# Kernel tuning notes

Hardware: AMD Instinct MI355X
Metric: run time of the kernel (lower is better)

The kernel has to match this reference:

```python
import jax, jax.numpy as jnp
import numpy as np

B, S, N_STATE, N_HEAD = 8, 4096, 1024, 16
N_FREQ = 10000.0
H_DIM = N_STATE // N_HEAD          # 64
N_ROTS = H_DIM // 2                # 32


def setup_inputs() -> dict:
    key = jax.random.key(0)
    k1, k2, k3, k4, k5 = jax.random.split(key, 5)
    x = jax.random.normal(k1, (B, S, N_STATE), dtype=jnp.float32)
    # rotation angles (module inits to zeros; small random values exercise the math)
    thetas = jax.random.normal(k2, (N_ROTS,), dtype=jnp.float32) * 0.1
    # r_pairs.long() in torch -> integer plane indices; ensure i != j
    i = jax.random.randint(k3, (N_ROTS,), 0, H_DIM)
    off = jax.random.randint(k4, (N_ROTS,), 1, H_DIM)
    j = (i + off) % H_DIM
    r_pairs = jnp.stack([i, j], axis=-1).astype(jnp.int32)
    theta_scale = jnp.ones((1,), dtype=jnp.float32)
    # r_matrix inits to identity; add small noise so it is non-trivial
    r_matrix = jnp.eye(H_DIM, dtype=jnp.float32) + 0.01 * jax.random.normal(k5, (H_DIM, H_DIM), dtype=jnp.float32)
    inv_freq = 1.0 / (N_FREQ ** (jnp.arange(0, H_DIM, 2, dtype=jnp.float32) / H_DIM))
    return {"x": x, "thetas": thetas, "theta_scale": theta_scale,
            "r_matrix": r_matrix, "inv_freq": inv_freq,
            "r_pairs": r_pairs, "n_head": N_HEAD}


def reference(x, thetas, theta_scale, r_matrix, inv_freq, r_pairs, n_head):
    b, s, n_state = x.shape
    h_dim = n_state // n_head
    x2d = x.reshape(-1, h_dim)  # [B*S*H, h_dim]
    angles = thetas * theta_scale[0]

    # Sequential Givens plane rotations: x @ G(i,j,theta) only touches columns i, j.
    def step(carry, inp):
        theta, ij = inp
        i, j = ij[0], ij[1]
        c, sn = jnp.cos(theta), jnp.sin(theta)
        xi = carry[:, i]
        xj = carry[:, j]
        carry = carry.at[:, i].set(xi * c + xj * sn)
        carry = carry.at[:, j].set(-xi * sn + xj * c)
        return carry, None

    x2d, _ = jax.lax.scan(step, x2d, (angles, r_pairs))
    x2d = x2d @ r_matrix
    xh = x2d.reshape(b, s, n_head, h_dim)

    # RoPE-style sin/cos mix
    pos = jnp.arange(s, dtype=jnp.float32)
    sinu = pos[:, None] * inv_freq[None, :]          # [s, h_dim//2]
    sin = jnp.sin(sinu)[None, :, None, :]
    cos = jnp.cos(sinu)[None, :, None, :]
    x1, x2 = xh[..., ::2], xh[..., 1::2]
    out = jnp.concatenate([x1 * cos - x2 * sin, x1 * sin + x2 * cos], axis=-1)
    return out.reshape(b, s, n_state)
```

## Files before the change

### kernel.cpp

```cpp
#include <hip/hip_runtime.h>
#include <cstdint>
#include <cstddef>

#define S_LEN   4096
#define NROT    32
#define NGRP    8192

typedef __attribute__((ext_vector_type(8))) short  short8x;
typedef __attribute__((ext_vector_type(4))) float  floatx4;

__device__ __host__ inline unsigned short f2bf(float f) {
  union { float f; unsigned u; } c; c.f = f;
  unsigned u = c.u;
  return (unsigned short)((u + 0x7fffu + ((u >> 16) & 1u)) >> 16);
}
__device__ inline float bf2f(unsigned short h) {
  union { unsigned u; float f; } c; c.u = ((unsigned)h) << 16;
  return c.f;
}

__global__ void setup_kernel(const float* __restrict__ thetas,
                             const float* __restrict__ theta_scale,
                             const float* __restrict__ r_matrix,
                             const int*   __restrict__ r_pairs,
                             const float* __restrict__ inv_freq,
                             uint4* __restrict__ Bfrag,
                             float* __restrict__ cosT,
                             float* __restrict__ sinT) {
  if (blockIdx.x < 512) {
    int idx = blockIdx.x * 256 + threadIdx.x;
    int s = idx >> 5;
    int f = idx & 31;
    float ang = (float)s * inv_freq[f];
    cosT[idx] = cosf(ang);
    sinT[idx] = sinf(ang);
    return;
  }
  __shared__ float C[64 * 65];
  __shared__ float Mm[64 * 64];
  int tid = threadIdx.x;
  if (tid < 64) {
    for (int c = 0; c < 64; ++c) C[tid * 65 + c] = (tid == c) ? 1.0f : 0.0f;
    float sc = theta_scale[0];
    for (int q = 0; q < NROT; ++q) {
      float th = thetas[q] * sc;
      float cs = cosf(th), sn = sinf(th);
      int i = r_pairs[2 * q], j = r_pairs[2 * q + 1];
      float xi = C[tid * 65 + i];
      float xj = C[tid * 65 + j];
      C[tid * 65 + i] =  xi * cs + xj * sn;
      C[tid * 65 + j] = -xi * sn + xj * cs;
    }
  }
  __syncthreads();
  for (int o = tid; o < 64 * 64; o += 256) {
    int t = o >> 6, c = o & 63;
    float a = 0.0f;
    for (int k = 0; k < 64; ++k) a = fmaf(C[t * 65 + k], r_matrix[k * 64 + c], a);
    Mm[o] = a;
  }
  __syncthreads();
  for (int e = tid; e < 16 * 64; e += 256) {
    int f = e >> 6, l = e & 63;
    int hl = f & 1, ks = (f >> 1) & 1, nt = f >> 2;
    int col = nt * 16 + (l & 15);
    unsigned short w[8];
    for (int j = 0; j < 8; ++j) {
      int k = ks * 32 + (l >> 4) * 8 + j;
      float m = Mm[k * 64 + col];
      unsigned short h = f2bf(m);
      if (hl == 0) w[j] = h;
      else         w[j] = f2bf(m - bf2f(h));
    }
    uint4 pk;
    pk.x = (unsigned)w[0] | ((unsigned)w[1] << 16);
    pk.y = (unsigned)w[2] | ((unsigned)w[3] << 16);
    pk.z = (unsigned)w[4] | ((unsigned)w[5] << 16);
    pk.w = (unsigned)w[6] | ((unsigned)w[7] << 16);
    Bfrag[e] = pk;
  }
}

__global__ __launch_bounds__(256)
void rotary_main(const float* __restrict__ x,
                 const uint4* __restrict__ Bfrag,
                 const float* __restrict__ cosT,
                 const float* __restrict__ sinT,
                 float* __restrict__ out) {
  __shared__ float obuf[4][1024];
  const int tid  = threadIdx.x;
  const int lane = tid & 63;
  const int wid  = tid >> 6;
  const int g    = blockIdx.x * 4 + wid;

  const short8x* Bp = (const short8x*)Bfrag;

  const int lr  = lane & 15;
  const int lk  = lane >> 4;
  const int dq  = lr >> 1;
  const int par = lane & 1;

  const float* xg = x + (size_t)g * 4096;
  float* og = out + (size_t)g * 4096;
  float* ob = &obuf[wid][0];

  floatx4 a[2][4];
  #define LOAD_A(mt, sl)                                                  \
    { const float* xr = xg + (size_t)((mt) * 16 + lr) * 64 + lk * 8;      \
      a[sl][0] = *(const floatx4*)(xr);                                   \
      a[sl][1] = *(const floatx4*)(xr + 4);                               \
      a[sl][2] = *(const floatx4*)(xr + 32);                              \
      a[sl][3] = *(const floatx4*)(xr + 36); }

  LOAD_A(0, 0)

  #pragma unroll
  for (int mt = 0; mt < 4; ++mt) {
    const int cur = mt & 1;
    short8x Ah0, Al0, Ah1, Al1;
    #pragma unroll
    for (int i = 0; i < 8; ++i) {
      float v0 = (i < 4) ? a[cur][0][i] : a[cur][1][i - 4];
      float v1 = (i < 4) ? a[cur][2][i] : a[cur][3][i - 4];
      unsigned short h0 = f2bf(v0);
      unsigned short h1 = f2bf(v1);
      Ah0[i] = (short)h0; Al0[i] = (short)f2bf(v0 - bf2f(h0));
      Ah1[i] = (short)h1; Al1[i] = (short)f2bf(v1 - bf2f(h1));
    }
    if (mt < 3) LOAD_A(mt + 1, (mt + 1) & 1)

    const int spos = (g * 4 + mt) & (S_LEN - 1);
    const float* ct = cosT + spos * 32;
    const float* st = sinT + spos * 32;

    #pragma unroll
    for (int nt = 0; nt < 4; ++nt) {
      short8x b0 = Bp[(nt * 4 + 0) * 64 + lane];
      short8x b1 = Bp[(nt * 4 + 1) * 64 + lane];
      short8x b2 = Bp[(nt * 4 + 2) * 64 + lane];
      short8x b3 = Bp[(nt * 4 + 3) * 64 + lane];

      floatx4 acc0 = {0.f, 0.f, 0.f, 0.f};
      floatx4 acc1 = {0.f, 0.f, 0.f, 0.f};
      acc0 = __builtin_amdgcn_mfma_f32_16x16x32_bf16(Ah0, b0, acc0, 0, 0, 0);
      acc1 = __builtin_amdgcn_mfma_f32_16x16x32_bf16(Ah1, b2, acc1, 0, 0, 0);
      acc0 = __builtin_amdgcn_mfma_f32_16x16x32_bf16(Ah0, b1, acc0, 0, 0, 0);
      acc1 = __builtin_amdgcn_mfma_f32_16x16x32_bf16(Ah1, b3, acc1, 0, 0, 0);
      acc0 = __builtin_amdgcn_mfma_f32_16x16x32_bf16(Al0, b0, acc0, 0, 0, 0);
      acc1 = __builtin_amdgcn_mfma_f32_16x16x32_bf16(Al1, b2, acc1, 0, 0, 0);

      const float cv = ct[nt * 8 + dq];
      const float sv = st[nt * 8 + dq];
      const int colout = par ? (32 + nt * 8 + dq) : (nt * 8 + dq);
      #pragma unroll
      for (int r = 0; r < 4; ++r) {
        float v = acc0[r] + acc1[r];
        float p = __shfl_xor(v, 1, 64);
        float o = par ? fmaf(p, sv, v * cv)
                      : fmaf(v, cv, -(p * sv));
        ob[(lk * 4 + r) * 64 + (colout ^ (lk << 3))] = o;
      }
    }

    asm volatile("s_waitcnt lgkmcnt(0)" ::: "memory");
    #pragma unroll
    for (int q = 0; q < 4; ++q) {
      const float* rp = ob + q * 256 + lk * 64 + ((lr * 4) ^ (q << 3));
      floatx4 vr = *(const floatx4*)rp;
      *(floatx4*)(og + (size_t)(mt * 16 + q * 4 + lk) * 64 + lr * 4) = vr;
    }
  }
  #undef LOAD_A
}

extern "C" void kernel_launch(void* const* d_in, const int* in_sizes, int n_in,
                              void* d_out, int out_size, void* d_ws, size_t ws_size,
                              hipStream_t stream) {
  const float* x           = (const float*)d_in[0];
  const float* thetas      = (const float*)d_in[1];
  const float* theta_scale = (const float*)d_in[2];
  const float* r_matrix    = (const float*)d_in[3];
  const float* inv_freq    = (const float*)d_in[4];
  const int*   r_pairs     = (const int*)d_in[5];

  uint4* Bfrag = (uint4*)d_ws;
  float* cosT  = (float*)d_ws + 4096;
  float* sinT  = cosT + S_LEN * 32;
  float* outp  = (float*)d_out;

  setup_kernel<<<513, 256, 0, stream>>>(thetas, theta_scale, r_matrix, r_pairs,
                                        inv_freq, Bfrag, cosT, sinT);
  rotary_main<<<NGRP / 4, 256, 0, stream>>>(x, Bfrag, cosT, sinT, outp);
}
```

Measured before the change: 82.23 us.

## Hoist B fragments into registers, double work per wave, interleave cos/sin table

Loads all 16 B-matrix MFMA fragments into registers once per wave instead of reloading them on every tile. Each wave now processes two 64-row groups (eight tiles), which halves the grid and amortizes the B loads. The cos and sin tables are merged into one float2 array so each lookup is a single load, and launch bounds request 3 blocks per SM. The cost is higher register pressure from 16 short8 fragments held in registers, and fewer blocks in flight for latency hiding in a memory-bound kernel.

New measurement: 91.33 us. 11.1% more time.

```diff
diff --git a/kernel.cpp b/kernel.cpp
--- a/kernel.cpp
+++ b/kernel.cpp
@@ -25,15 +25,13 @@
                              const int*   __restrict__ r_pairs,
                              const float* __restrict__ inv_freq,
                              uint4* __restrict__ Bfrag,
-                             float* __restrict__ cosT,
-                             float* __restrict__ sinT) {
+                             float2* __restrict__ csT) {
   if (blockIdx.x < 512) {
     int idx = blockIdx.x * 256 + threadIdx.x;
     int s = idx >> 5;
     int f = idx & 31;
     float ang = (float)s * inv_freq[f];
-    cosT[idx] = cosf(ang);
-    sinT[idx] = sinf(ang);
+    csT[idx] = make_float2(cosf(ang), sinf(ang));
     return;
   }
   __shared__ float C[64 * 65];
@@ -81,42 +79,43 @@
   }
 }
 
-__global__ __launch_bounds__(256)
+__global__ __launch_bounds__(256, 3)
 void rotary_main(const float* __restrict__ x,
                  const uint4* __restrict__ Bfrag,
-                 const float* __restrict__ cosT,
-                 const float* __restrict__ sinT,
+                 const float2* __restrict__ csT,
                  float* __restrict__ out) {
   __shared__ float obuf[4][1024];
   const int tid  = threadIdx.x;
   const int lane = tid & 63;
   const int wid  = tid >> 6;
-  const int g    = blockIdx.x * 4 + wid;
+  const int w    = blockIdx.x * 4 + wid;
 
   const short8x* Bp = (const short8x*)Bfrag;
+  short8x Bf[16];
+  #pragma unroll
+  for (int f = 0; f < 16; ++f) Bf[f] = Bp[f * 64 + lane];
 
   const int lr  = lane & 15;
   const int lk  = lane >> 4;
   const int dq  = lr >> 1;
   const int par = lane & 1;
 
-  const float* xg = x + (size_t)g * 4096;
-  float* og = out + (size_t)g * 4096;
   float* ob = &obuf[wid][0];
 
   floatx4 a[2][4];
-  #define LOAD_A(mt, sl)                                                  \
-    { const float* xr = xg + (size_t)((mt) * 16 + lr) * 64 + lk * 8;      \
-      a[sl][0] = *(const floatx4*)(xr);                                   \
-      a[sl][1] = *(const floatx4*)(xr + 4);                               \
-      a[sl][2] = *(const floatx4*)(xr + 32);                              \
+  #define LOAD_A(t, sl)                                                        \
+    { const float* xr = x + (size_t)(w * 2 + ((t) >> 2)) * 4096                \
+                          + (size_t)(((t) & 3) * 16 + lr) * 64 + lk * 8;       \
+      a[sl][0] = *(const floatx4*)(xr);                                        \
+      a[sl][1] = *(const floatx4*)(xr + 4);                                    \
+      a[sl][2] = *(const floatx4*)(xr + 32);                                   \
       a[sl][3] = *(const floatx4*)(xr + 36); }
 
   LOAD_A(0, 0)
 
   #pragma unroll
-  for (int mt = 0; mt < 4; ++mt) {
-    const int cur = mt & 1;
+  for (int t = 0; t < 8; ++t) {
+    const int cur = t & 1;
     short8x Ah0, Al0, Ah1, Al1;
     #pragma unroll
     for (int i = 0; i < 8; ++i) {
@@ -127,47 +126,42 @@
       Ah0[i] = (short)h0; Al0[i] = (short)f2bf(v0 - bf2f(h0));
       Ah1[i] = (short)h1; Al1[i] = (short)f2bf(v1 - bf2f(h1));
     }
-    if (mt < 3) LOAD_A(mt + 1, (mt + 1) & 1)
+    if (t < 7) LOAD_A(t + 1, (t + 1) & 1)
 
-    const int spos = (g * 4 + mt) & (S_LEN - 1);
-    const float* ct = cosT + spos * 32;
-    const float* st = sinT + spos * 32;
+    const int g    = w * 2 + (t >> 2);
+    const int spos = (g * 4 + (t & 3)) & (S_LEN - 1);
+    const float2* cst = csT + spos * 32;
 
     #pragma unroll
     for (int nt = 0; nt < 4; ++nt) {
-      short8x b0 = Bp[(nt * 4 + 0) * 64 + lane];
-      short8x b1 = Bp[(nt * 4 + 1) * 64 + lane];
-      short8x b2 = Bp[(nt * 4 + 2) * 64 + lane];
-      short8x b3 = Bp[(nt * 4 + 3) * 64 + lane];
-
       floatx4 acc0 = {0.f, 0.f, 0.f, 0.f};
       floatx4 acc1 = {0.f, 0.f, 0.f, 0.f};
-      acc0 = __builtin_amdgcn_mfma_f32_16x16x32_bf16(Ah0, b0, acc0, 0, 0, 0);
-      acc1 = __builtin_amdgcn_mfma_f32_16x16x32_bf16(Ah1, b2, acc1, 0, 0, 0);
-      acc0 = __builtin_amdgcn_mfma_f32_16x16x32_bf16(Ah0, b1, acc0, 0, 0, 0);
-      acc1 = __builtin_amdgcn_mfma_f32_16x16x32_bf16(Ah1, b3, acc1, 0, 0, 0);
-      acc0 = __builtin_amdgcn_mfma_f32_16x16x32_bf16(Al0, b0, acc0, 0, 0, 0);
-      acc1 = __builtin_amdgcn_mfma_f32_16x16x32_bf16(Al1, b2, acc1, 0, 0, 0);
+      acc0 = __builtin_amdgcn_mfma_f32_16x16x32_bf16(Ah0, Bf[nt * 4 + 0], acc0, 0, 0, 0);
+      acc1 = __builtin_amdgcn_mfma_f32_16x16x32_bf16(Ah1, Bf[nt * 4 + 2], acc1, 0, 0, 0);
+      acc0 = __builtin_amdgcn_mfma_f32_16x16x32_bf16(Ah0, Bf[nt * 4 + 1], acc0, 0, 0, 0);
+      acc1 = __builtin_amdgcn_mfma_f32_16x16x32_bf16(Ah1, Bf[nt * 4 + 3], acc1, 0, 0, 0);
+      acc0 = __builtin_amdgcn_mfma_f32_16x16x32_bf16(Al0, Bf[nt * 4 + 0], acc0, 0, 0, 0);
+      acc1 = __builtin_amdgcn_mfma_f32_16x16x32_bf16(Al1, Bf[nt * 4 + 2], acc1, 0, 0, 0);
 
-      const float cv = ct[nt * 8 + dq];
-      const float sv = st[nt * 8 + dq];
+      const float2 cs = cst[nt * 8 + dq];
       const int colout = par ? (32 + nt * 8 + dq) : (nt * 8 + dq);
       #pragma unroll
       for (int r = 0; r < 4; ++r) {
         float v = acc0[r] + acc1[r];
         float p = __shfl_xor(v, 1, 64);
-        float o = par ? fmaf(p, sv, v * cv)
-                      : fmaf(v, cv, -(p * sv));
+        float o = par ? fmaf(p, cs.y, v * cs.x)
+                      : fmaf(v, cs.x, -(p * cs.y));
         ob[(lk * 4 + r) * 64 + (colout ^ (lk << 3))] = o;
       }
     }
 
     asm volatile("s_waitcnt lgkmcnt(0)" ::: "memory");
+    float* og = out + (size_t)g * 4096;
     #pragma unroll
     for (int q = 0; q < 4; ++q) {
       const float* rp = ob + q * 256 + lk * 64 + ((lr * 4) ^ (q << 3));
       floatx4 vr = *(const floatx4*)rp;
-      *(floatx4*)(og + (size_t)(mt * 16 + q * 4 + lk) * 64 + lr * 4) = vr;
+      *(floatx4*)(og + (size_t)((t & 3) * 16 + q * 4 + lk) * 64 + lr * 4) = vr;
     }
   }
   #undef LOAD_A
@@ -183,12 +177,11 @@
   const float* inv_freq    = (const float*)d_in[4];
   const int*   r_pairs     = (const int*)d_in[5];
 
-  uint4* Bfrag = (uint4*)d_ws;
-  float* cosT  = (float*)d_ws + 4096;
-  float* sinT  = cosT + S_LEN * 32;
-  float* outp  = (float*)d_out;
+  uint4*  Bfrag = (uint4*)d_ws;
+  float2* csT   = (float2*)((char*)d_ws + 16384);
+  float*  outp  = (float*)d_out;
 
   setup_kernel<<<513, 256, 0, stream>>>(thetas, theta_scale, r_matrix, r_pairs,
-                                        inv_freq, Bfrag, cosT, sinT);
-  rotary_main<<<NGRP / 4, 256, 0, stream>>>(x, Bfrag, cosT, sinT, outp);
+                                        inv_freq, Bfrag, csT);
+  rotary_main<<<NGRP / 8, 256, 0, stream>>>(x, Bfrag, csT, outp);
 }
```
